# Kernel tuning notes

Hardware: AMD Instinct MI355X
Metric: run time of the kernel (lower is better)

Reference implementation:

```python
import jax, jax.numpy as jnp
import numpy as np

N, E, S, T, B, F = 50000, 150000, 32, 32, 64, 3
R = 1.1


def setup_inputs() -> dict:
    key = jax.random.key(0)
    k1, k2, k3, k4 = jax.random.split(key, 4)
    x = jax.random.normal(k1, (N, F), dtype=jnp.float32)
    # direction vectors, columns normalized (as in torch init)
    v = jax.random.uniform(k2, (T, F), dtype=jnp.float32) - 0.5
    v = (v / jnp.sqrt(jnp.sum(v * v, axis=1, keepdims=True))).T  # [F, T]
    lin = jnp.linspace(-R, R, S, dtype=jnp.float32)  # [S]
    edge_index = jax.random.randint(k3, (2, E), 0, N, dtype=jnp.int64)
    batch = jnp.sort(jax.random.randint(k4, (N,), 0, B, dtype=jnp.int64))
    return {"x": x, "v": v, "lin": lin, "edge_index": edge_index,
            "batch": batch, "num_graphs": B}


def _ecc_sum(h, idx, lin, num_graphs):
    # h: [M, T] heights, idx: [M] graph ids, lin: [S]
    # bump: sigmoid(50 * (lin - h)) -> [M, S, T]
    e = jax.nn.sigmoid(50.0 * (lin[None, :, None] - h[:, None, :]))
    return jax.ops.segment_sum(e, idx, num_segments=num_graphs)  # [B, S, T]


def reference(x, v, lin, edge_index, batch, num_graphs):
    nh = x @ v                                # [N, T] node heights
    eh = jnp.max(nh[edge_index], axis=0)      # [E, T] edge heights (max over endpoints)
    node_ect = _ecc_sum(nh, batch, lin, num_graphs)
    edge_ect = _ecc_sum(eh, batch[edge_index[0]], lin, num_graphs)
    return node_ect - edge_ect                # [B, S, T] == movedim(0,1) layout of torch
```

## Files before the change

kernel.cpp:

```cpp
#include <hip/hip_runtime.h>

#ifndef __has_builtin
#define __has_builtin(x) 0
#endif

__device__ __forceinline__ float fexp2(float x) {
#if __has_builtin(__builtin_amdgcn_exp2f)
    return __builtin_amdgcn_exp2f(x);
#else
    return exp2f(x);
#endif
}
__device__ __forceinline__ float frcp(float x) {
#if __has_builtin(__builtin_amdgcn_rcpf)
    return __builtin_amdgcn_rcpf(x);
#else
    return 1.0f / x;
#endif
}

constexpr int TT = 32;
constexpr int SS = 32;
constexpr int BB = 64;
constexpr int NB = 64;
constexpr int CPB_N = 8;
constexpr int CPB_E = 16;
constexpr float FL = 50.0f * 1.44269504088896340736f;
constexpr float QS = 65536.0f;
constexpr float IQS = 1.0f / 65536.0f;

__global__ __launch_bounds__(256) void prep_k(
    const int* __restrict__ batch, const int* __restrict__ src,
    int N, int E, int nB,
    int* __restrict__ starts, int* __restrict__ hist, float* __restrict__ out)
{
    if ((int)blockIdx.x < nB) {
        const int n = blockIdx.x * 256 + threadIdx.x;
        if (n >= N) return;
        const int g = batch[n];
        const int gp = (n == 0) ? -1 : batch[n - 1];
        for (int g2 = gp + 1; g2 <= g; ++g2) starts[g2] = n;
        if (n == N - 1)
            for (int g2 = g + 1; g2 <= BB; ++g2) starts[g2] = N;
    } else {
        const int b = blockIdx.x - nB;
        float4* o4 = (float4*)(out + (size_t)b * SS * TT);
        o4[threadIdx.x] = float4{0.f, 0.f, 0.f, 0.f};
        __shared__ int h[BB];
        if (threadIdx.x < BB) h[threadIdx.x] = 0;
        __syncthreads();
        const int per = (E + NB - 1) / NB;
        const int lo = b * per, hi = min(E, lo + per);
        for (int e = lo + threadIdx.x; e < hi; e += 256)
            atomicAdd(&h[batch[src[e]]], 1);
        __syncthreads();
        if (threadIdx.x < BB) hist[b * BB + threadIdx.x] = h[threadIdx.x];
    }
}

__device__ __forceinline__ void ect_core(
    const float* __restrict__ x, const float* __restrict__ v,
    const float* __restrict__ lin,
    const int* __restrict__ ssrc, const int* __restrict__ sdst,
    bool edge, int lo, int hi, int g, float sign, float* __restrict__ out)
{
    __shared__ unsigned accS[TT][SS + 1];
    __shared__ unsigned cntS[TT][SS + 1];
    __shared__ unsigned part[TT][9];
    for (int i = threadIdx.x; i < TT * (SS + 1); i += 256) {
        ((unsigned*)accS)[i] = 0u;
        ((unsigned*)cntS)[i] = 0u;
    }
    const int t = threadIdx.x & 31;
    const int pr = threadIdx.x >> 5;
    const float v0 = v[t], v1 = v[TT + t], v2 = v[2 * TT + t];
    const float l0 = lin[0];
    const float dS = lin[1] - l0;
    const float invD = frcp(dS);
    const float fld = FL * dS;
    const float pm1 = fexp2(fld), pp1 = fexp2(-fld);
    __syncthreads();

#pragma unroll 4
    for (int base = lo; base < hi; base += 8) {
        const int p = base + pr;
        if (p < hi) {
            float h;
            if (edge) {
                const int sn = ssrc[p], dn = sdst[p];
                const float hs = fmaf(x[3 * sn], v0, fmaf(x[3 * sn + 1], v1, x[3 * sn + 2] * v2));
                const float hd = fmaf(x[3 * dn], v0, fmaf(x[3 * dn + 1], v1, x[3 * dn + 2] * v2));
                h = fmaxf(hs, hd);
            } else {
                h = fmaf(x[3 * p], v0, fmaf(x[3 * p + 1], v1, x[3 * p + 2] * v2));
            }
            const float hl0 = h - l0;
            float fj = rintf(hl0 * invD);
            fj = fminf(34.f, fmaxf(-2.f, fj));
            const int j = (int)fj;
            const float delta = fmaf(-fj, dS, hl0);
            const float ucen = fexp2(FL * delta);
            const unsigned q0 = __float2uint_rn(QS * frcp(fmaf(ucen, pm1, 1.f)));
            const unsigned q1 = __float2uint_rn(QS * frcp(1.f + ucen));
            const unsigned q2 = __float2uint_rn(QS * frcp(fmaf(ucen, pp1, 1.f)));
            const int b = j + 2;
            if (b < SS) atomicAdd(&cntS[t][b], 1u);
            if (1 <= j && j <= SS) atomicAdd(&accS[t][j - 1], q0);
            if (0 <= j && j < SS)  atomicAdd(&accS[t][j], q1);
            if (-1 <= j && j < SS - 1) atomicAdd(&accS[t][j + 1], q2);
        }
    }
    __syncthreads();
    const unsigned c0 = cntS[t][4 * pr], c1 = cntS[t][4 * pr + 1];
    const unsigned c2 = cntS[t][4 * pr + 2], c3 = cntS[t][4 * pr + 3];
    part[t][pr + 1] = c0 + c1 + c2 + c3;
    if (pr == 0) part[t][0] = 0u;
    __syncthreads();
    if (pr == 0) {
        unsigned r = 0u;
#pragma unroll
        for (int q = 1; q <= 8; ++q) { r += part[t][q]; part[t][q] = r; }
    }
    __syncthreads();
    unsigned run = part[t][pr];
    float* o = out + (size_t)g * SS * TT;
    run += c0;
    atomicAdd(&o[(4 * pr + 0) * TT + t], sign * fmaf((float)accS[t][4 * pr + 0], IQS, (float)run));
    run += c1;
    atomicAdd(&o[(4 * pr + 1) * TT + t], sign * fmaf((float)accS[t][4 * pr + 1], IQS, (float)run));
    run += c2;
    atomicAdd(&o[(4 * pr + 2) * TT + t], sign * fmaf((float)accS[t][4 * pr + 2], IQS, (float)run));
    run += c3;
    atomicAdd(&o[(4 * pr + 3) * TT + t], sign * fmaf((float)accS[t][4 * pr + 3], IQS, (float)run));
}

__global__ __launch_bounds__(256) void mid_k(
    const float* __restrict__ x, const float* __restrict__ v,
    const float* __restrict__ lin,
    const int* __restrict__ src, const int* __restrict__ dst,
    const int* __restrict__ batch, int E,
    const int* __restrict__ hist, int* __restrict__ offs,
    int* __restrict__ ssrc, int* __restrict__ sdst,
    const int* __restrict__ starts, float* __restrict__ out)
{
    if ((int)blockIdx.x < NB) {
        __shared__ int lcur[BB];
        __shared__ int stot[BB];
        const int tid = threadIdx.x;
        if (tid < BB) {
            int accb = 0, tot = 0;
            for (int b = 0; b < NB; ++b) {
                const int hv = hist[b * BB + tid];
                accb += (b < (int)blockIdx.x) ? hv : 0;
                tot += hv;
            }
            lcur[tid] = accb;
            stot[tid] = tot;
        }
        __syncthreads();
        if (tid == 0) {
            int run = 0;
            for (int i = 0; i < BB; ++i) { const int tv = stot[i]; stot[i] = run; run += tv; }
            if (blockIdx.x == 0) offs[BB] = run;
        }
        __syncthreads();
        if (tid < BB) {
            lcur[tid] += stot[tid];
            if (blockIdx.x == 0) offs[tid] = stot[tid];
        }
        __syncthreads();
        const int per = (E + NB - 1) / NB;
        const int lo = blockIdx.x * per, hi = min(E, lo + per);
        for (int e = lo + tid; e < hi; e += 256) {
            const int s = src[e], d = dst[e];
            const int pos = atomicAdd(&lcur[batch[s]], 1);
            ssrc[pos] = s;
            sdst[pos] = d;
        }
    } else {
        const int bid = blockIdx.x - NB;
        const int g = bid / CPB_N, c = bid % CPB_N;
        const int s0 = starts[g], s1 = starts[g + 1];
        const int chunk = (s1 - s0 + CPB_N - 1) / CPB_N;
        const int lo = s0 + c * chunk;
        const int hi = min(s1, lo + chunk);
        ect_core(x, v, lin, nullptr, nullptr, false, lo, hi, g, 1.0f, out);
    }
}

__global__ __launch_bounds__(256) void edge_k(
    const float* __restrict__ x, const float* __restrict__ v,
    const float* __restrict__ lin,
    const int* __restrict__ ssrc, const int* __restrict__ sdst,
    const int* __restrict__ offs, float* __restrict__ out)
{
    const int g = blockIdx.x / CPB_E, c = blockIdx.x % CPB_E;
    const int s0 = offs[g], s1 = offs[g + 1];
    const int chunk = (s1 - s0 + CPB_E - 1) / CPB_E;
    const int lo = s0 + c * chunk;
    const int hi = min(s1, lo + chunk);
    ect_core(x, v, lin, ssrc, sdst, true, lo, hi, g, -1.0f, out);
}

extern "C" void kernel_launch(void* const* d_in, const int* in_sizes, int n_in,
                              void* d_out, int out_size, void* d_ws, size_t ws_size,
                              hipStream_t stream) {
    const float* x   = (const float*)d_in[0];
    const float* v   = (const float*)d_in[1];
    const float* lin = (const float*)d_in[2];
    const int* edge_index = (const int*)d_in[3];
    const int* batch = (const int*)d_in[4];

    const int N = in_sizes[0] / 3;
    const int E = in_sizes[3] / 2;
    const int* src = edge_index;
    const int* dst = edge_index + E;
    float* out = (float*)d_out;

    char* ws = (char*)d_ws;
    int* starts = (int*)ws;
    int* offs   = (int*)(ws + 512);
    int* hist   = (int*)(ws + 1024);
    int* ssrc   = (int*)(ws + 65536);
    int* sdst   = ssrc + E;

    const int nB = (N + 255) / 256;
    prep_k<<<nB + NB, 256, 0, stream>>>(batch, src, N, E, nB, starts, hist, out);
    mid_k<<<NB + BB * CPB_N, 256, 0, stream>>>(x, v, lin, src, dst, batch, E,
                                               hist, offs, ssrc, sdst, starts, out);
    edge_k<<<BB * CPB_E, 256, 0, stream>>>(x, v, lin, ssrc, sdst, offs, out);
}
```

Baseline: 34.33 us.

## Precompute node heights in prep kernel and pack sorted edge pairs as int2

Adds blocks to the prep kernel that compute all node heights x@v into a workspace table [N,32]. The node and edge ECT passes then read those heights instead of recomputing three-element dot products from x per edge endpoint. Sorted edge endpoints are also stored as a packed int2 instead of two separate arrays. This trades recomputation for an extra 6.4MB write and gathered 128B-row reads, which adds memory traffic that may or may not beat the cheap FMAs it removes.

```diff
diff --git a/kernel.cpp b/kernel.cpp
--- a/kernel.cpp
+++ b/kernel.cpp
@@ -25,14 +25,17 @@
 constexpr int NB = 64;
 constexpr int CPB_N = 8;
 constexpr int CPB_E = 16;
+constexpr int NHB = 256;
 constexpr float FL = 50.0f * 1.44269504088896340736f;
 constexpr float QS = 65536.0f;
 constexpr float IQS = 1.0f / 65536.0f;
 
 __global__ __launch_bounds__(256) void prep_k(
+    const float* __restrict__ x, const float* __restrict__ v,
     const int* __restrict__ batch, const int* __restrict__ src,
     int N, int E, int nB,
-    int* __restrict__ starts, int* __restrict__ hist, float* __restrict__ out)
+    int* __restrict__ starts, int* __restrict__ hist,
+    float* __restrict__ nh, float* __restrict__ out)
 {
     if ((int)blockIdx.x < nB) {
         const int n = blockIdx.x * 256 + threadIdx.x;
@@ -42,7 +45,7 @@
         for (int g2 = gp + 1; g2 <= g; ++g2) starts[g2] = n;
         if (n == N - 1)
             for (int g2 = g + 1; g2 <= BB; ++g2) starts[g2] = N;
-    } else {
+    } else if ((int)blockIdx.x < nB + NB) {
         const int b = blockIdx.x - nB;
         float4* o4 = (float4*)(out + (size_t)b * SS * TT);
         o4[threadIdx.x] = float4{0.f, 0.f, 0.f, 0.f};
@@ -55,13 +58,23 @@
             atomicAdd(&h[batch[src[e]]], 1);
         __syncthreads();
         if (threadIdx.x < BB) hist[b * BB + threadIdx.x] = h[threadIdx.x];
+    } else {
+        const int b = blockIdx.x - nB - NB;
+        const int t = threadIdx.x & 31, pr = threadIdx.x >> 5;
+        const float v0 = v[t], v1 = v[TT + t], v2 = v[2 * TT + t];
+        const int groups = (N + 7) / 8;
+        for (int grp = b; grp < groups; grp += NHB) {
+            const int p = grp * 8 + pr;
+            if (p < N)
+                nh[(p << 5) + t] =
+                    fmaf(x[3 * p], v0, fmaf(x[3 * p + 1], v1, x[3 * p + 2] * v2));
+        }
     }
 }
 
 __device__ __forceinline__ void ect_core(
-    const float* __restrict__ x, const float* __restrict__ v,
-    const float* __restrict__ lin,
-    const int* __restrict__ ssrc, const int* __restrict__ sdst,
+    const float* __restrict__ nh, const float* __restrict__ lin,
+    const int2* __restrict__ epair,
     bool edge, int lo, int hi, int g, float sign, float* __restrict__ out)
 {
     __shared__ unsigned accS[TT][SS + 1];
@@ -73,7 +86,6 @@
     }
     const int t = threadIdx.x & 31;
     const int pr = threadIdx.x >> 5;
-    const float v0 = v[t], v1 = v[TT + t], v2 = v[2 * TT + t];
     const float l0 = lin[0];
     const float dS = lin[1] - l0;
     const float invD = frcp(dS);
@@ -87,12 +99,10 @@
         if (p < hi) {
             float h;
             if (edge) {
-                const int sn = ssrc[p], dn = sdst[p];
-                const float hs = fmaf(x[3 * sn], v0, fmaf(x[3 * sn + 1], v1, x[3 * sn + 2] * v2));
-                const float hd = fmaf(x[3 * dn], v0, fmaf(x[3 * dn + 1], v1, x[3 * dn + 2] * v2));
-                h = fmaxf(hs, hd);
+                const int2 ed = epair[p];
+                h = fmaxf(nh[(ed.x << 5) + t], nh[(ed.y << 5) + t]);
             } else {
-                h = fmaf(x[3 * p], v0, fmaf(x[3 * p + 1], v1, x[3 * p + 2] * v2));
+                h = nh[(p << 5) + t];
             }
             const float hl0 = h - l0;
             float fj = rintf(hl0 * invD);
@@ -135,12 +145,11 @@
 }
 
 __global__ __launch_bounds__(256) void mid_k(
-    const float* __restrict__ x, const float* __restrict__ v,
-    const float* __restrict__ lin,
+    const float* __restrict__ nh, const float* __restrict__ lin,
     const int* __restrict__ src, const int* __restrict__ dst,
     const int* __restrict__ batch, int E,
     const int* __restrict__ hist, int* __restrict__ offs,
-    int* __restrict__ ssrc, int* __restrict__ sdst,
+    int2* __restrict__ epair,
     const int* __restrict__ starts, float* __restrict__ out)
 {
     if ((int)blockIdx.x < NB) {
@@ -174,8 +183,7 @@
         for (int e = lo + tid; e < hi; e += 256) {
             const int s = src[e], d = dst[e];
             const int pos = atomicAdd(&lcur[batch[s]], 1);
-            ssrc[pos] = s;
-            sdst[pos] = d;
+            epair[pos] = int2{s, d};
         }
     } else {
         const int bid = blockIdx.x - NB;
@@ -184,14 +192,13 @@
         const int chunk = (s1 - s0 + CPB_N - 1) / CPB_N;
         const int lo = s0 + c * chunk;
         const int hi = min(s1, lo + chunk);
-        ect_core(x, v, lin, nullptr, nullptr, false, lo, hi, g, 1.0f, out);
+        ect_core(nh, lin, nullptr, false, lo, hi, g, 1.0f, out);
     }
 }
 
 __global__ __launch_bounds__(256) void edge_k(
-    const float* __restrict__ x, const float* __restrict__ v,
-    const float* __restrict__ lin,
-    const int* __restrict__ ssrc, const int* __restrict__ sdst,
+    const float* __restrict__ nh, const float* __restrict__ lin,
+    const int2* __restrict__ epair,
     const int* __restrict__ offs, float* __restrict__ out)
 {
     const int g = blockIdx.x / CPB_E, c = blockIdx.x % CPB_E;
@@ -199,7 +206,7 @@
     const int chunk = (s1 - s0 + CPB_E - 1) / CPB_E;
     const int lo = s0 + c * chunk;
     const int hi = min(s1, lo + chunk);
-    ect_core(x, v, lin, ssrc, sdst, true, lo, hi, g, -1.0f, out);
+    ect_core(nh, lin, epair, true, lo, hi, g, -1.0f, out);
 }
 
 extern "C" void kernel_launch(void* const* d_in, const int* in_sizes, int n_in,
@@ -221,12 +228,14 @@
     int* starts = (int*)ws;
     int* offs   = (int*)(ws + 512);
     int* hist   = (int*)(ws + 1024);
-    int* ssrc   = (int*)(ws + 65536);
-    int* sdst   = ssrc + E;
+    int2* epair = (int2*)(ws + 65536);
+    float* nh   = (float*)(ws + 65536 +
+                           (((size_t)E * 8 + 255) / 256) * 256);
 
     const int nB = (N + 255) / 256;
-    prep_k<<<nB + NB, 256, 0, stream>>>(batch, src, N, E, nB, starts, hist, out);
-    mid_k<<<NB + BB * CPB_N, 256, 0, stream>>>(x, v, lin, src, dst, batch, E,
-                                               hist, offs, ssrc, sdst, starts, out);
-    edge_k<<<BB * CPB_E, 256, 0, stream>>>(x, v, lin, ssrc, sdst, offs, out);
-}
+    prep_k<<<nB + NB + NHB, 256, 0, stream>>>(x, v, batch, src, N, E, nB,
+                                              starts, hist, nh, out);
+    mid_k<<<NB + BB * CPB_N, 256, 0, stream>>>(nh, lin, src, dst, batch, E,
+                                               hist, offs, epair, starts, out);
+    edge_k<<<BB * CPB_E, 256, 0, stream>>>(nh, lin, epair, offs, out);
+}
```

Result: slower. 47.49 us (+38.3%).

## Replace edge bucket sort with per-block filtering over graph-id byte array

Applied to the files above, without the earlier changes.

Drops the histogram, prefix-scan and scatter passes that sorted edges by graph. A byte array of each edge's graph id is built instead, and every edge block scans its slice of all edges, compacting matching ones into a shared-memory queue before processing. The node and edge phases are merged into one kernel, cutting a launch and a dependency. In exchange, each block redundantly scans many non-matching edges and gathers src/dst indirectly through the queue.

```diff
diff --git a/kernel.cpp b/kernel.cpp
--- a/kernel.cpp
+++ b/kernel.cpp
@@ -22,9 +22,11 @@
 constexpr int TT = 32;
 constexpr int SS = 32;
 constexpr int BB = 64;
-constexpr int NB = 64;
 constexpr int CPB_N = 8;
 constexpr int CPB_E = 16;
+constexpr int ZB = 16;
+constexpr int GEB = 128;
+constexpr int QCAP = 2048;
 constexpr float FL = 50.0f * 1.44269504088896340736f;
 constexpr float QS = 65536.0f;
 constexpr float IQS = 1.0f / 65536.0f;
@@ -32,7 +34,8 @@
 __global__ __launch_bounds__(256) void prep_k(
     const int* __restrict__ batch, const int* __restrict__ src,
     int N, int E, int nB,
-    int* __restrict__ starts, int* __restrict__ hist, float* __restrict__ out)
+    int* __restrict__ starts, unsigned char* __restrict__ ge8,
+    float* __restrict__ out)
 {
     if ((int)blockIdx.x < nB) {
         const int n = blockIdx.x * 256 + threadIdx.x;
@@ -42,31 +45,30 @@
         for (int g2 = gp + 1; g2 <= g; ++g2) starts[g2] = n;
         if (n == N - 1)
             for (int g2 = g + 1; g2 <= BB; ++g2) starts[g2] = N;
+    } else if ((int)blockIdx.x < nB + ZB) {
+        float4* o4 = (float4*)out;
+        for (int i = (blockIdx.x - nB) * 256 + threadIdx.x; i < BB * SS * TT / 4;
+             i += ZB * 256)
+            o4[i] = float4{0.f, 0.f, 0.f, 0.f};
     } else {
-        const int b = blockIdx.x - nB;
-        float4* o4 = (float4*)(out + (size_t)b * SS * TT);
-        o4[threadIdx.x] = float4{0.f, 0.f, 0.f, 0.f};
-        __shared__ int h[BB];
-        if (threadIdx.x < BB) h[threadIdx.x] = 0;
-        __syncthreads();
-        const int per = (E + NB - 1) / NB;
-        const int lo = b * per, hi = min(E, lo + per);
-        for (int e = lo + threadIdx.x; e < hi; e += 256)
-            atomicAdd(&h[batch[src[e]]], 1);
-        __syncthreads();
-        if (threadIdx.x < BB) hist[b * BB + threadIdx.x] = h[threadIdx.x];
+        const int b = blockIdx.x - nB - ZB;
+        for (int e = b * 256 + threadIdx.x; e < E; e += GEB * 256)
+            ge8[e] = (unsigned char)batch[src[e]];
     }
 }
 
-__device__ __forceinline__ void ect_core(
+__global__ __launch_bounds__(256) void ect_k(
     const float* __restrict__ x, const float* __restrict__ v,
     const float* __restrict__ lin,
-    const int* __restrict__ ssrc, const int* __restrict__ sdst,
-    bool edge, int lo, int hi, int g, float sign, float* __restrict__ out)
+    const int* __restrict__ src, const int* __restrict__ dst,
+    const unsigned char* __restrict__ ge8,
+    const int* __restrict__ starts, int E, float* __restrict__ out)
 {
     __shared__ unsigned accS[TT][SS + 1];
     __shared__ unsigned cntS[TT][SS + 1];
     __shared__ unsigned part[TT][9];
+    __shared__ int q[QCAP];
+    __shared__ int qcnt;
     for (int i = threadIdx.x; i < TT * (SS + 1); i += 256) {
         ((unsigned*)accS)[i] = 0u;
         ((unsigned*)cntS)[i] = 0u;
@@ -81,33 +83,56 @@
     const float pm1 = fexp2(fld), pp1 = fexp2(-fld);
     __syncthreads();
 
-#pragma unroll 4
-    for (int base = lo; base < hi; base += 8) {
-        const int p = base + pr;
-        if (p < hi) {
-            float h;
-            if (edge) {
-                const int sn = ssrc[p], dn = sdst[p];
+    auto accum = [&](float h) {
+        const float hl0 = h - l0;
+        float fj = rintf(hl0 * invD);
+        fj = fminf(34.f, fmaxf(-2.f, fj));
+        const int j = (int)fj;
+        const float delta = fmaf(-fj, dS, hl0);
+        const float ucen = fexp2(FL * delta);
+        const unsigned q0 = __float2uint_rn(QS * frcp(fmaf(ucen, pm1, 1.f)));
+        const unsigned q1 = __float2uint_rn(QS * frcp(1.f + ucen));
+        const unsigned q2 = __float2uint_rn(QS * frcp(fmaf(ucen, pp1, 1.f)));
+        if (j + 2 < SS) atomicAdd(&cntS[t][j + 2], 1u);
+        if (1 <= j && j <= SS) atomicAdd(&accS[t][j - 1], q0);
+        if (0 <= j && j < SS)  atomicAdd(&accS[t][j], q1);
+        if (-1 <= j && j < SS - 1) atomicAdd(&accS[t][j + 1], q2);
+    };
+
+    const bool edge = blockIdx.x >= BB * CPB_N;
+    int g;
+    if (!edge) {
+        const int bid = blockIdx.x;
+        g = bid / CPB_N;
+        const int c = bid % CPB_N;
+        const int s0 = starts[g], s1 = starts[g + 1];
+        const int chunk = (s1 - s0 + CPB_N - 1) / CPB_N;
+        const int lo = s0 + c * chunk, hi = min(s1, lo + chunk);
+        for (int p = lo + pr; p < hi; p += 8)
+            accum(fmaf(x[3 * p], v0, fmaf(x[3 * p + 1], v1, x[3 * p + 2] * v2)));
+    } else {
+        const int bid = blockIdx.x - BB * CPB_N;
+        g = bid / CPB_E;
+        const int c = bid % CPB_E;
+        const int chunk = (E + CPB_E - 1) / CPB_E;
+        const int lo = c * chunk, hi = min(E, lo + chunk);
+        const unsigned char gg = (unsigned char)g;
+        for (int sub = lo; sub < hi; sub += QCAP) {
+            const int send = min(hi, sub + QCAP);
+            __syncthreads();
+            if (threadIdx.x == 0) qcnt = 0;
+            __syncthreads();
+            for (int e = sub + (int)threadIdx.x; e < send; e += 256)
+                if (ge8[e] == gg) { const int pos = atomicAdd(&qcnt, 1); q[pos] = e; }
+            __syncthreads();
+            const int nq = qcnt;
+            for (int i = pr; i < nq; i += 8) {
+                const int e = q[i];
+                const int sn = src[e], dn = dst[e];
                 const float hs = fmaf(x[3 * sn], v0, fmaf(x[3 * sn + 1], v1, x[3 * sn + 2] * v2));
                 const float hd = fmaf(x[3 * dn], v0, fmaf(x[3 * dn + 1], v1, x[3 * dn + 2] * v2));
-                h = fmaxf(hs, hd);
-            } else {
-                h = fmaf(x[3 * p], v0, fmaf(x[3 * p + 1], v1, x[3 * p + 2] * v2));
+                accum(fmaxf(hs, hd));
             }
-            const float hl0 = h - l0;
-            float fj = rintf(hl0 * invD);
-            fj = fminf(34.f, fmaxf(-2.f, fj));
-            const int j = (int)fj;
-            const float delta = fmaf(-fj, dS, hl0);
-            const float ucen = fexp2(FL * delta);
-            const unsigned q0 = __float2uint_rn(QS * frcp(fmaf(ucen, pm1, 1.f)));
-            const unsigned q1 = __float2uint_rn(QS * frcp(1.f + ucen));
-            const unsigned q2 = __float2uint_rn(QS * frcp(fmaf(ucen, pp1, 1.f)));
-            const int b = j + 2;
-            if (b < SS) atomicAdd(&cntS[t][b], 1u);
-            if (1 <= j && j <= SS) atomicAdd(&accS[t][j - 1], q0);
-            if (0 <= j && j < SS)  atomicAdd(&accS[t][j], q1);
-            if (-1 <= j && j < SS - 1) atomicAdd(&accS[t][j + 1], q2);
         }
     }
     __syncthreads();
@@ -119,10 +144,11 @@
     if (pr == 0) {
         unsigned r = 0u;
 #pragma unroll
-        for (int q = 1; q <= 8; ++q) { r += part[t][q]; part[t][q] = r; }
+        for (int qq = 1; qq <= 8; ++qq) { r += part[t][qq]; part[t][qq] = r; }
     }
     __syncthreads();
     unsigned run = part[t][pr];
+    const float sign = edge ? -1.f : 1.f;
     float* o = out + (size_t)g * SS * TT;
     run += c0;
     atomicAdd(&o[(4 * pr + 0) * TT + t], sign * fmaf((float)accS[t][4 * pr + 0], IQS, (float)run));
@@ -132,74 +158,6 @@
     atomicAdd(&o[(4 * pr + 2) * TT + t], sign * fmaf((float)accS[t][4 * pr + 2], IQS, (float)run));
     run += c3;
     atomicAdd(&o[(4 * pr + 3) * TT + t], sign * fmaf((float)accS[t][4 * pr + 3], IQS, (float)run));
-}
-
-__global__ __launch_bounds__(256) void mid_k(
-    const float* __restrict__ x, const float* __restrict__ v,
-    const float* __restrict__ lin,
-    const int* __restrict__ src, const int* __restrict__ dst,
-    const int* __restrict__ batch, int E,
-    const int* __restrict__ hist, int* __restrict__ offs,
-    int* __restrict__ ssrc, int* __restrict__ sdst,
-    const int* __restrict__ starts, float* __restrict__ out)
-{
-    if ((int)blockIdx.x < NB) {
-        __shared__ int lcur[BB];
-        __shared__ int stot[BB];
-        const int tid = threadIdx.x;
-        if (tid < BB) {
-            int accb = 0, tot = 0;
-            for (int b = 0; b < NB; ++b) {
-                const int hv = hist[b * BB + tid];
-                accb += (b < (int)blockIdx.x) ? hv : 0;
-                tot += hv;
-            }
-            lcur[tid] = accb;
-            stot[tid] = tot;
-        }
-        __syncthreads();
-        if (tid == 0) {
-            int run = 0;
-            for (int i = 0; i < BB; ++i) { const int tv = stot[i]; stot[i] = run; run += tv; }
-            if (blockIdx.x == 0) offs[BB] = run;
-        }
-        __syncthreads();
-        if (tid < BB) {
-            lcur[tid] += stot[tid];
-            if (blockIdx.x == 0) offs[tid] = stot[tid];
-        }
-        __syncthreads();
-        const int per = (E + NB - 1) / NB;
-        const int lo = blockIdx.x * per, hi = min(E, lo + per);
-        for (int e = lo + tid; e < hi; e += 256) {
-            const int s = src[e], d = dst[e];
-            const int pos = atomicAdd(&lcur[batch[s]], 1);
-            ssrc[pos] = s;
-            sdst[pos] = d;
-        }
-    } else {
-        const int bid = blockIdx.x - NB;
-        const int g = bid / CPB_N, c = bid % CPB_N;
-        const int s0 = starts[g], s1 = starts[g + 1];
-        const int chunk = (s1 - s0 + CPB_N - 1) / CPB_N;
-        const int lo = s0 + c * chunk;
-        const int hi = min(s1, lo + chunk);
-        ect_core(x, v, lin, nullptr, nullptr, false, lo, hi, g, 1.0f, out);
-    }
-}
-
-__global__ __launch_bounds__(256) void edge_k(
-    const float* __restrict__ x, const float* __restrict__ v,
-    const float* __restrict__ lin,
-    const int* __restrict__ ssrc, const int* __restrict__ sdst,
-    const int* __restrict__ offs, float* __restrict__ out)
-{
-    const int g = blockIdx.x / CPB_E, c = blockIdx.x % CPB_E;
-    const int s0 = offs[g], s1 = offs[g + 1];
-    const int chunk = (s1 - s0 + CPB_E - 1) / CPB_E;
-    const int lo = s0 + c * chunk;
-    const int hi = min(s1, lo + chunk);
-    ect_core(x, v, lin, ssrc, sdst, true, lo, hi, g, -1.0f, out);
 }
 
 extern "C" void kernel_launch(void* const* d_in, const int* in_sizes, int n_in,
@@ -218,15 +176,11 @@
     float* out = (float*)d_out;
 
     char* ws = (char*)d_ws;
-    int* starts = (int*)ws;
-    int* offs   = (int*)(ws + 512);
-    int* hist   = (int*)(ws + 1024);
-    int* ssrc   = (int*)(ws + 65536);
-    int* sdst   = ssrc + E;
+    int* starts        = (int*)ws;
+    unsigned char* ge8 = (unsigned char*)(ws + 512);
 
     const int nB = (N + 255) / 256;
-    prep_k<<<nB + NB, 256, 0, stream>>>(batch, src, N, E, nB, starts, hist, out);
-    mid_k<<<NB + BB * CPB_N, 256, 0, stream>>>(x, v, lin, src, dst, batch, E,
-                                               hist, offs, ssrc, sdst, starts, out);
-    edge_k<<<BB * CPB_E, 256, 0, stream>>>(x, v, lin, ssrc, sdst, offs, out);
+    prep_k<<<nB + ZB + GEB, 256, 0, stream>>>(batch, src, N, E, nB, starts, ge8, out);
+    ect_k<<<BB * (CPB_N + CPB_E), 256, 0, stream>>>(x, v, lin, src, dst, ge8,
+                                                    starts, E, out);
 }
```

After: 35.43 us. 3.2% more time.
